# Performance work log

Hardware: AMD Instinct MI355X
Metric: run time of the kernel (lower is better)

Reference implementation:

```python
import jax, jax.numpy as jnp
import numpy as np

N = 10000
E = 160000
NEG_SLOPE = 0.2
BN_EPS = 1e-5


def _gat_conv(x, W, a_src, a_dst, b, src, dst, n, heads):
    # PyG GATConv, concat=False (mean over heads), shared lin for src/dst.
    H = heads
    C = W.shape[1] // H
    h = (x @ W).reshape(n, H, C)                       # (N,H,C)
    e_s = jnp.einsum('nhc,hc->nh', h, a_src)           # (N,H)
    e_d = jnp.einsum('nhc,hc->nh', h, a_dst)
    alpha = jax.nn.leaky_relu(e_s[src] + e_d[dst], NEG_SLOPE)   # (E',H)
    amax = jax.ops.segment_max(alpha, dst, num_segments=n)       # per-dst softmax
    ex = jnp.exp(alpha - amax[dst])
    denom = jax.ops.segment_sum(ex, dst, num_segments=n)
    w = ex / (denom[dst] + 1e-16)
    out = jax.ops.segment_sum(h[src] * w[:, :, None], dst, num_segments=n)  # (N,H,C)
    return out.mean(axis=1) + b


def _bn(x, g, b):
    mu = x.mean(axis=0)
    var = x.var(axis=0)  # biased, as torch BN training forward
    return (x - mu) * jax.lax.rsqrt(var + BN_EPS) * g + b


def setup_inputs() -> dict:
    key = jax.random.key(0)
    ks = jax.random.split(key, 32)
    d = {}
    d['x'] = jax.random.normal(ks[0], (N, 64), jnp.float32)
    d['edge_index'] = jax.random.randint(ks[1], (2, E), 0, N, jnp.int64)
    s = lambda k, shape, fan: jax.random.normal(k, shape, jnp.float32) * (1.0 / np.sqrt(fan))
    d['Wp'] = s(ks[2], (64, 128), 64); d['bp'] = jnp.zeros((128,), jnp.float32)
    # conv0: 8 heads, per-head 128
    d['W0'] = s(ks[3], (128, 8 * 128), 128); d['as0'] = s(ks[4], (8, 128), 128)
    d['ad0'] = s(ks[5], (8, 128), 128); d['b0'] = jnp.zeros((128,), jnp.float32)
    d['g0'] = jnp.ones((128,), jnp.float32); d['be0'] = jnp.zeros((128,), jnp.float32)
    # conv1: same shape
    d['W1'] = s(ks[6], (128, 8 * 128), 128); d['as1'] = s(ks[7], (8, 128), 128)
    d['ad1'] = s(ks[8], (8, 128), 128); d['b1'] = jnp.zeros((128,), jnp.float32)
    d['g1'] = jnp.ones((128,), jnp.float32); d['be1'] = jnp.zeros((128,), jnp.float32)
    # conv2: 1 head, out 64
    d['W2'] = s(ks[9], (128, 64), 128); d['as2'] = s(ks[10], (1, 64), 64)
    d['ad2'] = s(ks[11], (1, 64), 64); d['b2'] = jnp.zeros((64,), jnp.float32)
    d['g2'] = jnp.ones((64,), jnp.float32); d['be2'] = jnp.zeros((64,), jnp.float32)
    # residual projection for layer 2 (128 -> 64)
    d['Wr'] = s(ks[12], (128, 64), 128); d['br'] = jnp.zeros((64,), jnp.float32)
    return d


def reference(x, edge_index, Wp, bp, W0, as0, ad0, b0, g0, be0,
              W1, as1, ad1, b1, g1, be1, W2, as2, ad2, b2, g2, be2, Wr, br):
    n = x.shape[0]
    loops = jnp.arange(n, dtype=edge_index.dtype)
    src = jnp.concatenate([edge_index[0], loops])  # add_self_loops=True
    dst = jnp.concatenate([edge_index[1], loops])
    h = x @ Wp + bp
    # layer 0 (8 heads, identity residual)
    hr = h
    h = jax.nn.elu(_bn(_gat_conv(h, W0, as0, ad0, b0, src, dst, n, 8), g0, be0)) + hr
    # layer 1
    hr = h
    h = jax.nn.elu(_bn(_gat_conv(h, W1, as1, ad1, b1, src, dst, n, 8), g1, be1)) + hr
    # layer 2 (1 head, linear residual 128->64)
    hr = h @ Wr + br
    h = jax.nn.elu(_bn(_gat_conv(h, W2, as2, ad2, b2, src, dst, n, 1), g2, be2)) + hr
    return h
```

## Files before the change

kernel.cpp:

```cpp
#include <hip/hip_runtime.h>
#include <hip/hip_bf16.h>
#include <cstdint>
#include <cstddef>

#define TPB 256

typedef __attribute__((ext_vector_type(8))) short bf16x8;
typedef __attribute__((ext_vector_type(8))) unsigned short ushort8;
typedef __attribute__((ext_vector_type(4))) float f32x4;
typedef __attribute__((ext_vector_type(8))) float f32x8;

static __device__ __forceinline__ float bf2f(unsigned short u) {
  union { unsigned int i; float f; } c;
  c.i = ((unsigned int)u) << 16;
  return c.f;
}

__global__ void detect_kernel(const unsigned int* __restrict__ w, int* __restrict__ flag) {
  __shared__ int any32;
  if (threadIdx.x == 0) any32 = 0;
  __syncthreads();
  for (int i = threadIdx.x; i < 1024; i += TPB)
    if (w[2 * i + 1] != 0u) any32 = 1;
  __syncthreads();
  if (threadIdx.x == 0) *flag = any32;
}

__global__ void decode_kernel(const void* __restrict__ raw, const int* __restrict__ flag,
                              int* __restrict__ src, int* __restrict__ dst, int E, int n) {
  int i = blockIdx.x * TPB + threadIdx.x;
  int tot = E + n;
  if (i >= tot) return;
  if (i < E) {
    if (*flag) {
      const int* p = (const int*)raw;
      src[i] = p[i];
      dst[i] = p[E + i];
    } else {
      const long long* p = (const long long*)raw;
      src[i] = (int)p[i];
      dst[i] = (int)p[E + i];
    }
  } else {
    src[i] = i - E;
    dst[i] = i - E;
  }
}

__global__ void count_kernel(const int* __restrict__ dst, int* __restrict__ counts, int etot) {
  int i = blockIdx.x * TPB + threadIdx.x;
  if (i < etot) atomicAdd(&counts[dst[i]], 1);
}

__global__ void scan_kernel(const int* __restrict__ counts, int* __restrict__ row_ptr, int n) {
  __shared__ int part[TPB];
  int tid = threadIdx.x;
  int chunk = (n + TPB - 1) / TPB;
  int begin = tid * chunk;
  int end = begin + chunk; if (end > n) end = n;
  int s = 0;
  for (int i = begin; i < end && i < n; i++) s += counts[i];
  part[tid] = s;
  __syncthreads();
  for (int off = 1; off < TPB; off <<= 1) {
    int v = (tid >= off) ? part[tid - off] : 0;
    __syncthreads();
    part[tid] += v;
    __syncthreads();
  }
  int base = (tid == 0) ? 0 : part[tid - 1];
  for (int i = begin; i < end && i < n; i++) { row_ptr[i] = base; base += counts[i]; }
  if (tid == TPB - 1) row_ptr[n] = base;
}

__global__ void fill_kernel(const int* __restrict__ src, const int* __restrict__ dst,
                            const int* __restrict__ row_ptr, int* __restrict__ fill,
                            int* __restrict__ sorted_src, int etot) {
  int i = blockIdx.x * TPB + threadIdx.x;
  if (i >= etot) return;
  int d = dst[i];
  int pos = row_ptr[d] + atomicAdd(&fill[d], 1);
  sorted_src[pos] = src[i];
}

__global__ void f32_to_bf16_kernel(const float* __restrict__ in, __hip_bfloat16* __restrict__ out, int n) {
  int i = blockIdx.x * TPB + threadIdx.x;
  if (i < n) out[i] = __float2bfloat16(in[i]);
}

__global__ void f32_to_bf16_T_kernel(const float* __restrict__ in, __hip_bfloat16* __restrict__ out,
                                     int K, int N) {
  __shared__ float tile[32][33];
  const int k0 = blockIdx.x * 32, n0 = blockIdx.y * 32;
  const int tx = threadIdx.x & 31, ty = threadIdx.x >> 5;
  for (int r = ty; r < 32; r += 8) {
    int k = k0 + r, n = n0 + tx;
    tile[r][tx] = (k < K && n < N) ? in[(size_t)k * N + n] : 0.f;
  }
  __syncthreads();
  for (int r = ty; r < 32; r += 8) {
    int n = n0 + r, k = k0 + tx;
    if (n < N && k < K) out[(size_t)n * K + k] = __float2bfloat16(tile[tx][r]);
  }
}

__global__ __launch_bounds__(256) void gemm_bf16t_kernel(
    const short* __restrict__ A, const short* __restrict__ Bt,
    const float* __restrict__ bias, float* __restrict__ C,
    __hip_bfloat16* __restrict__ Cb, int M, int N, int K) {
  __shared__ short As[64][40];
  __shared__ short Bs[128][40];

  const int tid = threadIdx.x;
  const int lane = tid & 63;
  const int w = tid >> 6;
  const int bm = blockIdx.x * 64;
  const int bn = blockIdx.y * 128;

  f32x4 acc[8];
#pragma unroll
  for (int nt = 0; nt < 8; nt++) acc[nt] = (f32x4){0.f, 0.f, 0.f, 0.f};

  const int arow = tid >> 2;
  const int akk = (tid & 3) << 3;
  const int brow = tid >> 1;
  const int bkk = (tid & 1) << 4;

  for (int k0 = 0; k0 < K; k0 += 32) {
    {
      int gr = bm + arow;
      if (gr < M) {
        *(bf16x8*)&As[arow][akk] = *(const bf16x8*)&A[(size_t)gr * K + k0 + akk];
      } else {
        bf16x8 z = {0, 0, 0, 0, 0, 0, 0, 0};
        *(bf16x8*)&As[arow][akk] = z;
      }
    }
    {
      int gbn = bn + brow;
      if (gbn < N) {
        const short* bp = &Bt[(size_t)gbn * K + k0 + bkk];
        *(bf16x8*)&Bs[brow][bkk]     = *(const bf16x8*)bp;
        *(bf16x8*)&Bs[brow][bkk + 8] = *(const bf16x8*)(bp + 8);
      } else {
        bf16x8 z = {0, 0, 0, 0, 0, 0, 0, 0};
        *(bf16x8*)&Bs[brow][bkk] = z;
        *(bf16x8*)&Bs[brow][bkk + 8] = z;
      }
    }
    __syncthreads();

    bf16x8 a = *(const bf16x8*)&As[w * 16 + (lane & 15)][(lane >> 4) * 8];
#pragma unroll
    for (int nt = 0; nt < 8; nt++) {
      bf16x8 b = *(const bf16x8*)&Bs[nt * 16 + (lane & 15)][(lane >> 4) * 8];
      acc[nt] = __builtin_amdgcn_mfma_f32_16x16x32_bf16(a, b, acc[nt], 0, 0, 0);
    }
    __syncthreads();
  }

#pragma unroll
  for (int nt = 0; nt < 8; nt++) {
    int gc = bn + nt * 16 + (lane & 15);
    if (gc >= N) continue;
    float bv = bias ? bias[gc] : 0.f;
#pragma unroll
    for (int q = 0; q < 4; q++) {
      int gr = bm + w * 16 + (lane >> 4) * 4 + q;
      if (gr < M) {
        float val = acc[nt][q] + bv;
        if (C) C[(size_t)gr * N + gc] = val;
        if (Cb) Cb[(size_t)gr * N + gc] = __float2bfloat16(val);
      }
    }
  }
}

__global__ void attn_coeff8_kernel(const unsigned short* __restrict__ gb,
                                   const float* __restrict__ asrc,
                                   const float* __restrict__ adst,
                                   float* __restrict__ es, float* __restrict__ ed) {
  const int v = blockIdx.x;
  const int tid = threadIdx.x;
  ushort4 gu = *(const ushort4*)&gb[(size_t)v * 1024 + 4 * tid];
  float4 av = *(const float4*)&asrc[4 * tid];
  float4 dv = *(const float4*)&adst[4 * tid];
  float gx = bf2f(gu.x), gy = bf2f(gu.y), gz = bf2f(gu.z), gw = bf2f(gu.w);
  float p1 = gx * av.x + gy * av.y + gz * av.z + gw * av.w;
  float p2 = gx * dv.x + gy * dv.y + gz * dv.z + gw * dv.w;
#pragma unroll
  for (int off = 16; off > 0; off >>= 1) {
    p1 += __shfl_down(p1, off);
    p2 += __shfl_down(p2, off);
  }
  if ((tid & 31) == 0) {
    es[(size_t)v * 8 + (tid >> 5)] = p1;
    ed[(size_t)v * 8 + (tid >> 5)] = p2;
  }
}

template <int H, int C>
__global__ void attn_coeff_kernel(const float* __restrict__ g,
                                  const float* __restrict__ asrc,
                                  const float* __restrict__ adst,
                                  float* __restrict__ es, float* __restrict__ ed) {
  int v = blockIdx.x;
  int tid = threadIdx.x;
  __shared__ float rs[2], rd[2];
  const float* grow = g + (size_t)v * (H * C);
  for (int h = 0; h < H; ++h) {
    float gv = grow[h * C + tid];
    float p1 = gv * asrc[h * C + tid];
    float p2 = gv * adst[h * C + tid];
#pragma unroll
    for (int off = 32; off > 0; off >>= 1) {
      p1 += __shfl_down(p1, off);
      p2 += __shfl_down(p2, off);
    }
    if ((tid & 63) == 0) { rs[tid >> 6] = p1; rd[tid >> 6] = p2; }
    __syncthreads();
    if (tid == 0) {
      float s1 = rs[0], s2 = rd[0];
      if (C > 64) { s1 += rs[1]; s2 += rd[1]; }
      es[(size_t)v * H + h] = s1;
      ed[(size_t)v * H + h] = s2;
    }
    __syncthreads();
  }
}

__global__ __launch_bounds__(256) void gat_aggregate8_kernel(
    const int* __restrict__ row_ptr, const int* __restrict__ srcs,
    const unsigned short* __restrict__ gb, const float* __restrict__ es,
    const float* __restrict__ ed, const float* __restrict__ bias,
    float* __restrict__ out) {
  constexpr int T = 256, H = 8, HC = 1024, CAP = 128;
  const int v = blockIdx.x;
  const int tid = threadIdx.x;
  const int h = tid & 7;
  const int jj = tid >> 3;

  __shared__ float alds[CAP * H];
  __shared__ int slds[CAP];
  __shared__ float red[T];
  __shared__ float mh[H], invd[H], edv8[H];
  __shared__ float red8[T][8];

  const int begin = row_ptr[v];
  const int deg = row_ptr[v + 1] - begin;

  if (tid < H) edv8[tid] = ed[(size_t)v * H + tid];
  __syncthreads();

  const int half = tid >> 7;
  const int t128 = tid & 127;
  const int c0 = t128 * 8;
  const int hh = t128 >> 4;

  f32x8 acc = {0.f, 0.f, 0.f, 0.f, 0.f, 0.f, 0.f, 0.f};

  auto gather = [&](int cnt) {
    int j = half;
    for (; j + 6 < cnt; j += 8) {
      int s0 = slds[j], s1 = slds[j + 2], s2 = slds[j + 4], s3 = slds[j + 6];
      float w0 = alds[j * 8 + hh], w1 = alds[(j + 2) * 8 + hh];
      float w2 = alds[(j + 4) * 8 + hh], w3 = alds[(j + 6) * 8 + hh];
      ushort8 u0 = *(const ushort8*)&gb[(size_t)s0 * HC + c0];
      ushort8 u1 = *(const ushort8*)&gb[(size_t)s1 * HC + c0];
      ushort8 u2 = *(const ushort8*)&gb[(size_t)s2 * HC + c0];
      ushort8 u3 = *(const ushort8*)&gb[(size_t)s3 * HC + c0];
#pragma unroll
      for (int k = 0; k < 8; k++)
        acc[k] += w0 * bf2f(u0[k]) + w1 * bf2f(u1[k]) + w2 * bf2f(u2[k]) + w3 * bf2f(u3[k]);
    }
    for (; j < cnt; j += 2) {
      int s = slds[j];
      float wv = alds[j * 8 + hh];
      ushort8 u = *(const ushort8*)&gb[(size_t)s * HC + c0];
#pragma unroll
      for (int k = 0; k < 8; k++) acc[k] += wv * bf2f(u[k]);
    }
  };

  if (deg <= CAP) {
    for (int idx = tid; idx < deg * 8; idx += T) {
      int j = idx >> 3, hx = idx & 7;
      int s = srcs[begin + j];
      if (hx == 0) slds[j] = s;
      float a = es[(size_t)s * 8 + hx] + edv8[hx];
      alds[idx] = a > 0.f ? a : 0.2f * a;
    }
    __syncthreads();
    float pm = -1e30f;
    for (int j = jj; j < deg; j += 32) pm = fmaxf(pm, alds[j * 8 + h]);
    red[tid] = pm;
    __syncthreads();
    if (tid < H) {
      float m = -1e30f;
      for (int g2 = 0; g2 < 32; g2++) m = fmaxf(m, red[g2 * 8 + tid]);
      mh[tid] = m;
    }
    __syncthreads();
    float ps = 0.f;
    float m = mh[h];
    for (int j = jj; j < deg; j += 32) {
      float p = __expf(alds[j * 8 + h] - m);
      alds[j * 8 + h] = p;
      ps += p;
    }
    red[tid] = ps;
    __syncthreads();
    if (tid < H) {
      float d = 0.f;
      for (int g2 = 0; g2 < 32; g2++) d += red[g2 * 8 + tid];
      invd[tid] = 1.0f / (d + 1e-16f);
    }
    __syncthreads();
    for (int idx = tid; idx < deg * 8; idx += T) alds[idx] *= invd[idx & 7];
    __syncthreads();
    gather(deg);
  } else {
    float pm = -1e30f;
    for (int j = jj; j < deg; j += 32) {
      int s = srcs[begin + j];
      float a = es[(size_t)s * 8 + h] + edv8[h];
      a = a > 0.f ? a : 0.2f * a;
      pm = fmaxf(pm, a);
    }
    red[tid] = pm;
    __syncthreads();
    if (tid < H) {
      float m = -1e30f;
      for (int g2 = 0; g2 < 32; g2++) m = fmaxf(m, red[g2 * 8 + tid]);
      mh[tid] = m;
    }
    __syncthreads();
    float ps = 0.f;
    for (int j = jj; j < deg; j += 32) {
      int s = srcs[begin + j];
      float a = es[(size_t)s * 8 + h] + edv8[h];
      a = a > 0.f ? a : 0.2f * a;
      ps += __expf(a - mh[h]);
    }
    red[tid] = ps;
    __syncthreads();
    if (tid < H) {
      float d = 0.f;
      for (int g2 = 0; g2 < 32; g2++) d += red[g2 * 8 + tid];
      invd[tid] = 1.0f / (d + 1e-16f);
    }
    for (int base = 0; base < deg; base += CAP) {
      int cnt = deg - base; if (cnt > CAP) cnt = CAP;
      __syncthreads();
      for (int idx = tid; idx < cnt * 8; idx += T) {
        int j = idx >> 3, hx = idx & 7;
        int s = srcs[begin + base + j];
        if (hx == 0) slds[j] = s;
        float a = es[(size_t)s * 8 + hx] + edv8[hx];
        a = a > 0.f ? a : 0.2f * a;
        alds[idx] = __expf(a - mh[hx]) * invd[hx];
      }
      __syncthreads();
      gather(cnt);
    }
  }

  __syncthreads();
#pragma unroll
  for (int k = 0; k < 8; k++) red8[tid][k] = acc[k];
  __syncthreads();
  if (tid < 16) {
    float o[8] = {0.f, 0.f, 0.f, 0.f, 0.f, 0.f, 0.f, 0.f};
    for (int q = 0; q < 16; q++) {
      const float* r = red8[q * 16 + tid];
#pragma unroll
      for (int k = 0; k < 8; k++) o[k] += r[k];
    }
    int cb = tid * 8;
#pragma unroll
    for (int k = 0; k < 8; k++)
      out[(size_t)v * 128 + cb + k] = o[k] * 0.125f + bias[cb + k];
  }
}

__global__ __launch_bounds__(256) void gat_aggregate1_kernel(
    const int* __restrict__ row_ptr, const int* __restrict__ srcs,
    const float* __restrict__ g, const float* __restrict__ es,
    const float* __restrict__ ed, const float* __restrict__ bias,
    float* __restrict__ out, int n) {
  const int wave = threadIdx.x >> 6;
  const int lane = threadIdx.x & 63;
  const int v = blockIdx.x * 4 + wave;
  if (v >= n) return;

  const int begin = row_ptr[v];
  const int deg = row_ptr[v + 1] - begin;
  const float edv = ed[v];

  float pm = -1e30f;
  for (int j = lane; j < deg; j += 64) {
    float a = es[srcs[begin + j]] + edv;
    a = a > 0.f ? a : 0.2f * a;
    pm = fmaxf(pm, a);
  }
#pragma unroll
  for (int off = 32; off > 0; off >>= 1) pm = fmaxf(pm, __shfl_xor(pm, off));

  float ps = 0.f;
  for (int j = lane; j < deg; j += 64) {
    float a = es[srcs[begin + j]] + edv;
    a = a > 0.f ? a : 0.2f * a;
    ps += expf(a - pm);
  }
#pragma unroll
  for (int off = 32; off > 0; off >>= 1) ps += __shfl_xor(ps, off);
  const float invd = 1.0f / (ps + 1e-16f);

  float acc = 0.f;
  for (int base = 0; base < deg; base += 64) {
    int cnt = deg - base; if (cnt > 64) cnt = 64;
    int sv = 0; float wv = 0.f;
    if (lane < cnt) {
      sv = srcs[begin + base + lane];
      float a = es[sv] + edv;
      a = a > 0.f ? a : 0.2f * a;
      wv = expf(a - pm) * invd;
    }
    for (int j = 0; j < cnt; j++) {
      int s = __shfl(sv, j);
      float wgt = __shfl(wv, j);
      acc += wgt * g[(size_t)s * 64 + lane];
    }
  }
  out[(size_t)v * 64 + lane] = acc + bias[lane];
}

template <int C>
__global__ void bn_stats_kernel(const float* __restrict__ x, int n, float* __restrict__ sums) {
  constexpr int T = 256;
  constexpr int RPI = T / C;
  constexpr int ITER = 64;
  constexpr int ROWS = RPI * ITER;
  int c = threadIdx.x % C;
  int r0 = threadIdx.x / C;
  int rowBase = blockIdx.x * ROWS;
  float s = 0.f, q = 0.f;
  for (int it = 0; it < ITER; ++it) {
    int r = rowBase + it * RPI + r0;
    if (r < n) {
      float v = x[(size_t)r * C + c];
      s += v; q += v * v;
    }
  }
  __shared__ float ls[T], lq[T];
  ls[threadIdx.x] = s; lq[threadIdx.x] = q;
  __syncthreads();
  if (threadIdx.x < C) {
    float ts = 0.f, tq = 0.f;
    for (int r = 0; r < RPI; ++r) { ts += ls[c + r * C]; tq += lq[c + r * C]; }
    atomicAdd(&sums[c], ts);
    atomicAdd(&sums[C + c], tq);
  }
}

template <int C>
__global__ void bn_elu_res_kernel(const float* __restrict__ x, const float* __restrict__ sums,
                                  const float* __restrict__ gamma, const float* __restrict__ beta,
                                  const float* __restrict__ res, float* __restrict__ out,
                                  __hip_bfloat16* __restrict__ outb, int n) {
  int i = blockIdx.x * TPB + threadIdx.x;
  if (i >= n * C) return;
  int c = i % C;
  float inv_n = 1.0f / (float)n;
  float mu = sums[c] * inv_n;
  float var = sums[C + c] * inv_n - mu * mu;
  float y = (x[i] - mu) * rsqrtf(var + 1e-5f) * gamma[c] + beta[c];
  y = y > 0.f ? y : expm1f(y);
  y += res[i];
  out[i] = y;
  if (outb) outb[i] = __float2bfloat16(y);
}

extern "C" void kernel_launch(void* const* d_in, const int* in_sizes, int n_in,
                              void* d_out, int out_size, void* d_ws, size_t ws_size,
                              hipStream_t stream) {
  const float* x   = (const float*)d_in[0];
  const void*  ei  = d_in[1];
  const float* Wp  = (const float*)d_in[2];
  const float* bp  = (const float*)d_in[3];
  const float* W0  = (const float*)d_in[4];
  const float* as0 = (const float*)d_in[5];
  const float* ad0 = (const float*)d_in[6];
  const float* b0  = (const float*)d_in[7];
  const float* g0  = (const float*)d_in[8];
  const float* be0 = (const float*)d_in[9];
  const float* W1  = (const float*)d_in[10];
  const float* as1 = (const float*)d_in[11];
  const float* ad1 = (const float*)d_in[12];
  const float* b1  = (const float*)d_in[13];
  const float* g1  = (const float*)d_in[14];
  const float* be1 = (const float*)d_in[15];
  const float* W2  = (const float*)d_in[16];
  const float* as2 = (const float*)d_in[17];
  const float* ad2 = (const float*)d_in[18];
  const float* b2  = (const float*)d_in[19];
  const float* g2  = (const float*)d_in[20];
  const float* be2 = (const float*)d_in[21];
  const float* Wr  = (const float*)d_in[22];
  const float* br  = (const float*)d_in[23];

  const int N = in_sizes[0] / 64;
  const int E = in_sizes[1] / 2;
  const int ETOT = E + N;

  char* wsp = (char*)d_ws;
  size_t off = 0;
  auto alloc = [&](size_t bytes) -> void* {
    void* p = wsp + off;
    off += (bytes + 255) & ~(size_t)255;
    return p;
  };
  int*   flag    = (int*)alloc(4);
  int*   e_src   = (int*)alloc((size_t)ETOT * 4);
  int*   e_dst   = (int*)alloc((size_t)ETOT * 4);
  int*   counts  = (int*)alloc((size_t)N * 4);
  int*   fillc   = (int*)alloc((size_t)N * 4);
  int*   row_ptr = (int*)alloc((size_t)(N + 1) * 4);
  int*   s_src   = (int*)alloc((size_t)ETOT * 4);
  float* hA      = (float*)alloc((size_t)N * 128 * 4);
  float* hB      = (float*)alloc((size_t)N * 128 * 4);
  float* gbuf    = (float*)alloc((size_t)N * 64 * 4);
  float* gat     = (float*)alloc((size_t)N * 128 * 4);
  float* es      = (float*)alloc((size_t)N * 8 * 4);
  float* ed      = (float*)alloc((size_t)N * 8 * 4);
  float* bnsum   = (float*)alloc(2 * 128 * 4);
  __hip_bfloat16* gbufb = (__hip_bfloat16*)alloc((size_t)N * 1024 * 2);
  __hip_bfloat16* xb  = (__hip_bfloat16*)alloc((size_t)N * 64 * 2);
  __hip_bfloat16* hAb = (__hip_bfloat16*)alloc((size_t)N * 128 * 2);
  __hip_bfloat16* hBb = (__hip_bfloat16*)alloc((size_t)N * 128 * 2);
  __hip_bfloat16* WpT = (__hip_bfloat16*)alloc((size_t)128 * 64 * 2);
  __hip_bfloat16* W0T = (__hip_bfloat16*)alloc((size_t)1024 * 128 * 2);
  __hip_bfloat16* W1T = (__hip_bfloat16*)alloc((size_t)1024 * 128 * 2);
  __hip_bfloat16* W2T = (__hip_bfloat16*)alloc((size_t)64 * 128 * 2);
  __hip_bfloat16* WrT = (__hip_bfloat16*)alloc((size_t)64 * 128 * 2);

  const int egrid = (ETOT + TPB - 1) / TPB;
  const int mgrid = (N + 63) / 64;
  auto cgrid = [](int n) { return (n + TPB - 1) / TPB; };

  detect_kernel<<<1, TPB, 0, stream>>>((const unsigned int*)ei, flag);
  decode_kernel<<<egrid, TPB, 0, stream>>>(ei, flag, e_src, e_dst, E, N);
  hipMemsetAsync(counts, 0, (size_t)N * 4, stream);
  hipMemsetAsync(fillc, 0, (size_t)N * 4, stream);
  count_kernel<<<egrid, TPB, 0, stream>>>(e_dst, counts, ETOT);
  scan_kernel<<<1, TPB, 0, stream>>>(counts, row_ptr, N);
  fill_kernel<<<egrid, TPB, 0, stream>>>(e_src, e_dst, row_ptr, fillc, s_src, ETOT);

  f32_to_bf16_kernel<<<cgrid(N * 64), TPB, 0, stream>>>(x, xb, N * 64);
  f32_to_bf16_T_kernel<<<dim3(2, 4), 256, 0, stream>>>(Wp, WpT, 64, 128);
  f32_to_bf16_T_kernel<<<dim3(4, 32), 256, 0, stream>>>(W0, W0T, 128, 1024);
  f32_to_bf16_T_kernel<<<dim3(4, 32), 256, 0, stream>>>(W1, W1T, 128, 1024);
  f32_to_bf16_T_kernel<<<dim3(4, 2), 256, 0, stream>>>(W2, W2T, 128, 64);
  f32_to_bf16_T_kernel<<<dim3(4, 2), 256, 0, stream>>>(Wr, WrT, 128, 64);

  gemm_bf16t_kernel<<<dim3(mgrid, 1), 256, 0, stream>>>(
      (const short*)xb, (const short*)WpT, bp, hA, hAb, N, 128, 64);

  gemm_bf16t_kernel<<<dim3(mgrid, 8), 256, 0, stream>>>(
      (const short*)hAb, (const short*)W0T, nullptr, nullptr, gbufb, N, 1024, 128);
  attn_coeff8_kernel<<<N, 256, 0, stream>>>((const unsigned short*)gbufb, as0, ad0, es, ed);
  gat_aggregate8_kernel<<<N, 256, 0, stream>>>(row_ptr, s_src, (const unsigned short*)gbufb, es, ed, b0, gat);
  hipMemsetAsync(bnsum, 0, 2 * 128 * 4, stream);
  bn_stats_kernel<128><<<(N + 127) / 128, 256, 0, stream>>>(gat, N, bnsum);
  bn_elu_res_kernel<128><<<cgrid(N * 128), TPB, 0, stream>>>(gat, bnsum, g0, be0, hA, hB, hBb, N);

  gemm_bf16t_kernel<<<dim3(mgrid, 8), 256, 0, stream>>>(
      (const short*)hBb, (const short*)W1T, nullptr, nullptr, gbufb, N, 1024, 128);
  attn_coeff8_kernel<<<N, 256, 0, stream>>>((const unsigned short*)gbufb, as1, ad1, es, ed);
  gat_aggregate8_kernel<<<N, 256, 0, stream>>>(row_ptr, s_src, (const unsigned short*)gbufb, es, ed, b1, gat);
  hipMemsetAsync(bnsum, 0, 2 * 128 * 4, stream);
  bn_stats_kernel<128><<<(N + 127) / 128, 256, 0, stream>>>(gat, N, bnsum);
  bn_elu_res_kernel<128><<<cgrid(N * 128), TPB, 0, stream>>>(gat, bnsum, g1, be1, hB, hA, hAb, N);

  gemm_bf16t_kernel<<<dim3(mgrid, 1), 256, 0, stream>>>(
      (const short*)hAb, (const short*)WrT, br, hB, nullptr, N, 64, 128);
  gemm_bf16t_kernel<<<dim3(mgrid, 1), 256, 0, stream>>>(
      (const short*)hAb, (const short*)W2T, nullptr, gbuf, nullptr, N, 64, 128);
  attn_coeff_kernel<1, 64><<<N, 64, 0, stream>>>(gbuf, as2, ad2, es, ed);
  gat_aggregate1_kernel<<<(N + 3) / 4, 256, 0, stream>>>(row_ptr, s_src, gbuf, es, ed, b2, gat, N);
  hipMemsetAsync(bnsum, 0, 2 * 64 * 4, stream);
  bn_stats_kernel<64><<<(N + 255) / 256, 256, 0, stream>>>(gat, N, bnsum);
  bn_elu_res_kernel<64><<<cgrid(N * 64), TPB, 0, stream>>>(gat, bnsum, g2, be2, hB, (float*)d_out, nullptr, N);
}
```

Before: 340.9 us.

## Aggregate 8-head GAT with one wavefront per node using shuffle softmax

```diff
diff --git a/kernel.cpp b/kernel.cpp
--- a/kernel.cpp
+++ b/kernel.cpp
@@ -8,7 +8,6 @@
 typedef __attribute__((ext_vector_type(8))) short bf16x8;
 typedef __attribute__((ext_vector_type(8))) unsigned short ushort8;
 typedef __attribute__((ext_vector_type(4))) float f32x4;
-typedef __attribute__((ext_vector_type(8))) float f32x8;
 
 static __device__ __forceinline__ float bf2f(unsigned short u) {
   union { unsigned int i; float f; } c;
@@ -229,157 +228,144 @@
   }
 }
 
-__global__ __launch_bounds__(256) void gat_aggregate8_kernel(
+__global__ __launch_bounds__(256) void gat_aggregate8w_kernel(
     const int* __restrict__ row_ptr, const int* __restrict__ srcs,
     const unsigned short* __restrict__ gb, const float* __restrict__ es,
     const float* __restrict__ ed, const float* __restrict__ bias,
-    float* __restrict__ out) {
-  constexpr int T = 256, H = 8, HC = 1024, CAP = 128;
-  const int v = blockIdx.x;
-  const int tid = threadIdx.x;
-  const int h = tid & 7;
-  const int jj = tid >> 3;
-
-  __shared__ float alds[CAP * H];
-  __shared__ int slds[CAP];
-  __shared__ float red[T];
-  __shared__ float mh[H], invd[H], edv8[H];
-  __shared__ float red8[T][8];
+    float* __restrict__ out, int n) {
+  const int wave = threadIdx.x >> 6;
+  const int lane = threadIdx.x & 63;
+  const int v = blockIdx.x * 4 + wave;
+  if (v >= n) return;
 
   const int begin = row_ptr[v];
   const int deg = row_ptr[v + 1] - begin;
 
-  if (tid < H) edv8[tid] = ed[(size_t)v * H + tid];
-  __syncthreads();
-
-  const int half = tid >> 7;
-  const int t128 = tid & 127;
-  const int c0 = t128 * 8;
-  const int hh = t128 >> 4;
-
-  f32x8 acc = {0.f, 0.f, 0.f, 0.f, 0.f, 0.f, 0.f, 0.f};
-
-  auto gather = [&](int cnt) {
-    int j = half;
-    for (; j + 6 < cnt; j += 8) {
-      int s0 = slds[j], s1 = slds[j + 2], s2 = slds[j + 4], s3 = slds[j + 6];
-      float w0 = alds[j * 8 + hh], w1 = alds[(j + 2) * 8 + hh];
-      float w2 = alds[(j + 4) * 8 + hh], w3 = alds[(j + 6) * 8 + hh];
-      ushort8 u0 = *(const ushort8*)&gb[(size_t)s0 * HC + c0];
-      ushort8 u1 = *(const ushort8*)&gb[(size_t)s1 * HC + c0];
-      ushort8 u2 = *(const ushort8*)&gb[(size_t)s2 * HC + c0];
-      ushort8 u3 = *(const ushort8*)&gb[(size_t)s3 * HC + c0];
-#pragma unroll
-      for (int k = 0; k < 8; k++)
-        acc[k] += w0 * bf2f(u0[k]) + w1 * bf2f(u1[k]) + w2 * bf2f(u2[k]) + w3 * bf2f(u3[k]);
-    }
-    for (; j < cnt; j += 2) {
-      int s = slds[j];
-      float wv = alds[j * 8 + hh];
-      ushort8 u = *(const ushort8*)&gb[(size_t)s * HC + c0];
-#pragma unroll
-      for (int k = 0; k < 8; k++) acc[k] += wv * bf2f(u[k]);
-    }
-  };
-
-  if (deg <= CAP) {
-    for (int idx = tid; idx < deg * 8; idx += T) {
-      int j = idx >> 3, hx = idx & 7;
-      int s = srcs[begin + j];
-      if (hx == 0) slds[j] = s;
-      float a = es[(size_t)s * 8 + hx] + edv8[hx];
-      alds[idx] = a > 0.f ? a : 0.2f * a;
-    }
-    __syncthreads();
-    float pm = -1e30f;
-    for (int j = jj; j < deg; j += 32) pm = fmaxf(pm, alds[j * 8 + h]);
-    red[tid] = pm;
-    __syncthreads();
-    if (tid < H) {
-      float m = -1e30f;
-      for (int g2 = 0; g2 < 32; g2++) m = fmaxf(m, red[g2 * 8 + tid]);
-      mh[tid] = m;
-    }
-    __syncthreads();
-    float ps = 0.f;
-    float m = mh[h];
-    for (int j = jj; j < deg; j += 32) {
-      float p = __expf(alds[j * 8 + h] - m);
-      alds[j * 8 + h] = p;
-      ps += p;
-    }
-    red[tid] = ps;
-    __syncthreads();
-    if (tid < H) {
-      float d = 0.f;
-      for (int g2 = 0; g2 < 32; g2++) d += red[g2 * 8 + tid];
-      invd[tid] = 1.0f / (d + 1e-16f);
-    }
-    __syncthreads();
-    for (int idx = tid; idx < deg * 8; idx += T) alds[idx] *= invd[idx & 7];
-    __syncthreads();
-    gather(deg);
+  const int eh = lane & 7;
+  const int ee = lane >> 3;
+  const int hh = lane >> 3;
+  const int c0 = lane << 4;
+
+  const float edv = ed[(size_t)v * 8 + eh];
+
+  float acc[16];
+#pragma unroll
+  for (int k = 0; k < 16; k++) acc[k] = 0.f;
+
+  if (deg <= 64) {
+    float a[8];
+    int sreg[8];
+#pragma unroll
+    for (int b = 0; b < 8; b++) {
+      a[b] = -1e30f;
+      sreg[b] = 0;
+      int e = b * 8 + ee;
+      if (e < deg) {
+        int s = srcs[begin + e];
+        sreg[b] = s;
+        float t = es[(size_t)s * 8 + eh] + edv;
+        a[b] = t > 0.f ? t : 0.2f * t;
+      }
+    }
+    float m = a[0];
+#pragma unroll
+    for (int b = 1; b < 8; b++) m = fmaxf(m, a[b]);
+    m = fmaxf(m, __shfl_xor(m, 8));
+    m = fmaxf(m, __shfl_xor(m, 16));
+    m = fmaxf(m, __shfl_xor(m, 32));
+    float dsum = 0.f;
+#pragma unroll
+    for (int b = 0; b < 8; b++) { a[b] = __expf(a[b] - m); dsum += a[b]; }
+    dsum += __shfl_xor(dsum, 8);
+    dsum += __shfl_xor(dsum, 16);
+    dsum += __shfl_xor(dsum, 32);
+    const float invd = 1.0f / (dsum + 1e-16f);
+#pragma unroll
+    for (int b = 0; b < 8; b++) a[b] *= invd;
+
+#pragma unroll
+    for (int b = 0; b < 8; b++) {
+      if (b * 8 >= deg) break;
+#pragma unroll
+      for (int jj = 0; jj < 8; jj++) {
+        if (b * 8 + jj >= deg) break;
+        const int sl = (jj << 3) | hh;
+        const int s = __shfl(sreg[b], sl);
+        const float w = __shfl(a[b], sl);
+        const ushort8* p = (const ushort8*)&gb[(size_t)s * 1024 + c0];
+        ushort8 u0 = p[0], u1 = p[1];
+#pragma unroll
+        for (int k = 0; k < 8; k++) {
+          acc[k]     += w * bf2f(u0[k]);
+          acc[k + 8] += w * bf2f(u1[k]);
+        }
+      }
+    }
   } else {
-    float pm = -1e30f;
-    for (int j = jj; j < deg; j += 32) {
-      int s = srcs[begin + j];
-      float a = es[(size_t)s * 8 + h] + edv8[h];
-      a = a > 0.f ? a : 0.2f * a;
-      pm = fmaxf(pm, a);
-    }
-    red[tid] = pm;
-    __syncthreads();
-    if (tid < H) {
-      float m = -1e30f;
-      for (int g2 = 0; g2 < 32; g2++) m = fmaxf(m, red[g2 * 8 + tid]);
-      mh[tid] = m;
-    }
-    __syncthreads();
-    float ps = 0.f;
-    for (int j = jj; j < deg; j += 32) {
-      int s = srcs[begin + j];
-      float a = es[(size_t)s * 8 + h] + edv8[h];
-      a = a > 0.f ? a : 0.2f * a;
-      ps += __expf(a - mh[h]);
-    }
-    red[tid] = ps;
-    __syncthreads();
-    if (tid < H) {
-      float d = 0.f;
-      for (int g2 = 0; g2 < 32; g2++) d += red[g2 * 8 + tid];
-      invd[tid] = 1.0f / (d + 1e-16f);
-    }
-    for (int base = 0; base < deg; base += CAP) {
-      int cnt = deg - base; if (cnt > CAP) cnt = CAP;
-      __syncthreads();
-      for (int idx = tid; idx < cnt * 8; idx += T) {
-        int j = idx >> 3, hx = idx & 7;
-        int s = srcs[begin + base + j];
-        if (hx == 0) slds[j] = s;
-        float a = es[(size_t)s * 8 + hx] + edv8[hx];
-        a = a > 0.f ? a : 0.2f * a;
-        alds[idx] = __expf(a - mh[hx]) * invd[hx];
-      }
-      __syncthreads();
-      gather(cnt);
-    }
-  }
-
-  __syncthreads();
-#pragma unroll
-  for (int k = 0; k < 8; k++) red8[tid][k] = acc[k];
-  __syncthreads();
-  if (tid < 16) {
-    float o[8] = {0.f, 0.f, 0.f, 0.f, 0.f, 0.f, 0.f, 0.f};
-    for (int q = 0; q < 16; q++) {
-      const float* r = red8[q * 16 + tid];
-#pragma unroll
-      for (int k = 0; k < 8; k++) o[k] += r[k];
-    }
-    int cb = tid * 8;
-#pragma unroll
-    for (int k = 0; k < 8; k++)
-      out[(size_t)v * 128 + cb + k] = o[k] * 0.125f + bias[cb + k];
+    float m = -1e30f;
+    for (int base = 0; base < deg; base += 8) {
+      int e = base + ee;
+      if (e < deg) {
+        int s = srcs[begin + e];
+        float t = es[(size_t)s * 8 + eh] + edv;
+        t = t > 0.f ? t : 0.2f * t;
+        m = fmaxf(m, t);
+      }
+    }
+    m = fmaxf(m, __shfl_xor(m, 8));
+    m = fmaxf(m, __shfl_xor(m, 16));
+    m = fmaxf(m, __shfl_xor(m, 32));
+    float dsum = 0.f;
+    for (int base = 0; base < deg; base += 8) {
+      int e = base + ee;
+      if (e < deg) {
+        int s = srcs[begin + e];
+        float t = es[(size_t)s * 8 + eh] + edv;
+        t = t > 0.f ? t : 0.2f * t;
+        dsum += __expf(t - m);
+      }
+    }
+    dsum += __shfl_xor(dsum, 8);
+    dsum += __shfl_xor(dsum, 16);
+    dsum += __shfl_xor(dsum, 32);
+    const float invd = 1.0f / (dsum + 1e-16f);
+    for (int base = 0; base < deg; base += 8) {
+      int e = base + ee;
+      float w = 0.f; int s = 0;
+      if (e < deg) {
+        s = srcs[begin + e];
+        float t = es[(size_t)s * 8 + eh] + edv;
+        t = t > 0.f ? t : 0.2f * t;
+        w = __expf(t - m) * invd;
+      }
+#pragma unroll
+      for (int jj = 0; jj < 8; jj++) {
+        if (base + jj >= deg) break;
+        const int sl = (jj << 3) | hh;
+        const int ss = __shfl(s, sl);
+        const float ww = __shfl(w, sl);
+        const ushort8* p = (const ushort8*)&gb[(size_t)ss * 1024 + c0];
+        ushort8 u0 = p[0], u1 = p[1];
+#pragma unroll
+        for (int k = 0; k < 8; k++) {
+          acc[k]     += ww * bf2f(u0[k]);
+          acc[k + 8] += ww * bf2f(u1[k]);
+        }
+      }
+    }
+  }
+
+#pragma unroll
+  for (int k = 0; k < 16; k++) {
+    acc[k] += __shfl_xor(acc[k], 8);
+    acc[k] += __shfl_xor(acc[k], 16);
+    acc[k] += __shfl_xor(acc[k], 32);
+  }
+  if (hh == 0) {
+    const int cc = (lane & 7) << 4;
+#pragma unroll
+    for (int k = 0; k < 16; k++)
+      out[(size_t)v * 128 + cc + k] = acc[k] * 0.125f + bias[cc + k];
   }
 }
 
@@ -569,7 +555,8 @@
   gemm_bf16t_kernel<<<dim3(mgrid, 8), 256, 0, stream>>>(
       (const short*)hAb, (const short*)W0T, nullptr, nullptr, gbufb, N, 1024, 128);
   attn_coeff8_kernel<<<N, 256, 0, stream>>>((const unsigned short*)gbufb, as0, ad0, es, ed);
-  gat_aggregate8_kernel<<<N, 256, 0, stream>>>(row_ptr, s_src, (const unsigned short*)gbufb, es, ed, b0, gat);
+  gat_aggregate8w_kernel<<<(N + 3) / 4, 256, 0, stream>>>(
+      row_ptr, s_src, (const unsigned short*)gbufb, es, ed, b0, gat, N);
   hipMemsetAsync(bnsum, 0, 2 * 128 * 4, stream);
   bn_stats_kernel<128><<<(N + 127) / 128, 256, 0, stream>>>(gat, N, bnsum);
   bn_elu_res_kernel<128><<<cgrid(N * 128), TPB, 0, stream>>>(gat, bnsum, g0, be0, hA, hB, hBb, N);
@@ -577,7 +564,8 @@
   gemm_bf16t_kernel<<<dim3(mgrid, 8), 256, 0, stream>>>(
       (const short*)hBb, (const short*)W1T, nullptr, nullptr, gbufb, N, 1024, 128);
   attn_coeff8_kernel<<<N, 256, 0, stream>>>((const unsigned short*)gbufb, as1, ad1, es, ed);
-  gat_aggregate8_kernel<<<N, 256, 0, stream>>>(row_ptr, s_src, (const unsigned short*)gbufb, es, ed, b1, gat);
+  gat_aggregate8w_kernel<<<(N + 3) / 4, 256, 0, stream>>>(
+      row_ptr, s_src, (const unsigned short*)gbufb, es, ed, b1, gat, N);
   hipMemsetAsync(bnsum, 0, 2 * 128 * 4, stream);
   bn_stats_kernel<128><<<(N + 127) / 128, 256, 0, stream>>>(gat, N, bnsum);
   bn_elu_res_kernel<128><<<cgrid(N * 128), TPB, 0, stream>>>(gat, bnsum, g1, be1, hB, hA, hAb, N);
```

Measured after the change: 336.0 us. No clear change (-1.4%).
